# Kernel optimization log

Measured on AMD Instinct MI355X. Metric: run time of the kernel, lower is better.

The kernel has to match this reference:

```python
import jax, jax.numpy as jnp
import numpy as np

B, D, C = 8192, 256, 128
MARGIN = 0.5
REPULSION_WEIGHT = 1.0
ALPHA = 0.5
BETA = 0.5
EPS = 1e-6  # F.pairwise_distance default eps, added to the difference vector


def make_centers(num_classes=C, embedding_dim=D):
    # center[k] is +/-1 one-hot along axis (k % embedding_dim)
    idx = np.arange(num_classes)
    centers = np.zeros((num_classes, embedding_dim), dtype=np.float32)
    centers[idx, idx % embedding_dim] = np.where(idx % 2 == 0, 1.0, -1.0)
    return jnp.asarray(centers)


def setup_inputs() -> dict:
    key = jax.random.key(0)
    k1, k2, k3 = jax.random.split(key, 3)
    features = jax.random.normal(k1, (B, D), dtype=jnp.float32)
    classification = jax.random.normal(k2, (B, C), dtype=jnp.float32)
    labels = jax.random.randint(k3, (B,), 0, C, dtype=jnp.int32)
    return {"features": features, "classification": classification, "labels": labels}


def _sculpted_loss(embeddings, labels, centers):
    b = embeddings.shape[0]
    # attractive: MSE to per-sample class center, mean over all elements
    center_targets = centers[labels]  # [B, D]
    attractive = jnp.mean((embeddings - center_targets) ** 2)

    # repulsive: for pairs i<j with different labels,
    # relu(margin - ||e_i - e_j + eps||_2)^2, summed then / (B(B-1)/2).
    sq_norm = jnp.sum(embeddings ** 2, axis=1)          # [B]
    row_sum = jnp.sum(embeddings, axis=1)               # [B]
    gram = embeddings @ embeddings.T                    # [B, B]
    sq = (sq_norm[:, None] + sq_norm[None, :] - 2.0 * gram
          + 2.0 * EPS * (row_sum[:, None] - row_sum[None, :])
          + embeddings.shape[1] * (EPS * EPS))
    dist = jnp.sqrt(jnp.maximum(sq, 1e-12))             # [B, B]

    iu = jnp.triu(jnp.ones((b, b), dtype=bool), k=1)    # i < j
    diff_label = labels[:, None] != labels[None, :]
    mask = iu & diff_label
    hinge = jnp.maximum(MARGIN - dist, 0.0)
    repulsive = jnp.sum(jnp.where(mask, hinge * hinge, 0.0))
    repulsive = repulsive / (b * (b - 1) / 2.0)

    return attractive + REPULSION_WEIGHT * repulsive


def reference(features, classification, labels):
    centers = make_centers()
    # cross entropy (mean over batch)
    logp = jax.nn.log_softmax(classification, axis=-1)
    ce = -jnp.mean(jnp.take_along_axis(logp, labels[:, None].astype(jnp.int32), axis=1)[:, 0])
    contrastive = _sculpted_loss(features, labels, centers)
    return BETA * contrastive + ALPHA * ce
```

## Files before the change

kernel.cpp:

```cpp
#include <hip/hip_runtime.h>
#include <stdint.h>

#define B_N   8192
#define D_DIM 256
#define C_CLS 128
#define EPSV  1e-6f
#define DEPS  (256.0f * EPSV * EPSV)
#define NT    64
#define NTRI  (NT * (NT + 1) / 2)

typedef __bf16 bf16x8 __attribute__((ext_vector_type(8)));
typedef float  f32x4  __attribute__((ext_vector_type(4)));

__device__ __forceinline__ unsigned short f2bf(float v) {
    unsigned u = __float_as_uint(v);
    u += 0x7fff + ((u >> 16) & 1);
    return (unsigned short)(u >> 16);
}


__global__ __launch_bounds__(256) void k_prep(
        const float* __restrict__ feat, const float* __restrict__ cls,
        const int* __restrict__ labels, unsigned short* __restrict__ ebf,
        float* __restrict__ aR, float* __restrict__ bC,
        float* __restrict__ attrP, float* __restrict__ ceP) {
    int t = threadIdx.x, lane = t & 63, w = t >> 6;
    int row = blockIdx.x * 4 + w;
    int lab = labels[row];

    const float4* src = (const float4*)(feat + (size_t)row * D_DIM);
    float4 f = src[lane];
    ushort4 p;
    p.x = f2bf(f.x); p.y = f2bf(f.y); p.z = f2bf(f.z); p.w = f2bf(f.w);
    ((ushort4*)(ebf + (size_t)row * D_DIM))[lane] = p;

    float sq = f.x*f.x + f.y*f.y + f.z*f.z + f.w*f.w;
    float sm = f.x + f.y + f.z + f.w;
    float arr[4] = {f.x, f.y, f.z, f.w};
    float pick = ((lab >> 2) == lane) ? arr[lab & 3] : 0.f;

    const float2* csrc = (const float2*)(cls + (size_t)row * C_CLS);
    float2 c2 = csrc[lane];
    float mx = fmaxf(c2.x, c2.y);
    #pragma unroll
    for (int off = 32; off; off >>= 1) mx = fmaxf(mx, __shfl_xor(mx, off));
    float es = expf(c2.x - mx) + expf(c2.y - mx);
    float cpick = ((lab >> 1) == lane) ? ((lab & 1) ? c2.y : c2.x) : 0.f;

    #pragma unroll
    for (int off = 32; off; off >>= 1) {
        sq    += __shfl_xor(sq, off);
        sm    += __shfl_xor(sm, off);
        pick  += __shfl_xor(pick, off);
        es    += __shfl_xor(es, off);
        cpick += __shfl_xor(cpick, off);
    }
    __shared__ float wsumA[4], wsumC[4];
    if (lane == 0) {
        aR[row] = sq + 2.f * EPSV * sm;
        bC[row] = sq - 2.f * EPSV * sm + DEPS;
        float s = (lab & 1) ? -1.f : 1.f;
        wsumA[w] = sq - 2.f * s * pick + 1.f;
        wsumC[w] = -(cpick - mx - logf(es));
    }
    __syncthreads();
    if (t == 0) {
        attrP[blockIdx.x] = wsumA[0] + wsumA[1] + wsumA[2] + wsumA[3];
        ceP[blockIdx.x]   = wsumC[0] + wsumC[1] + wsumC[2] + wsumC[3];
    }
}

__global__ __launch_bounds__(256) void k_gram(
        const unsigned short* __restrict__ ebf, const float* __restrict__ aR,
        const float* __restrict__ bC, const int* __restrict__ labels,
        float* __restrict__ repP) {
    __shared__ __align__(16) unsigned short As[128 * 128];
    __shared__ __align__(16) unsigned short Bs[128 * 128];
    __shared__ float aM[128], bN[128];
    __shared__ int   lM[128], lN[128];
    __shared__ float wred[4];

    int t = threadIdx.x, lane = t & 63, w = t >> 6;

    int bid = blockIdx.x, tm = 0;
    while (bid >= NT - tm) { bid -= NT - tm; tm++; }
    int tn = tm + bid;

    if (t < 128) {
        int i = tm * 128 + t;
        aM[t] = aR[i]; lM[t] = labels[i];
    } else {
        int j = tn * 128 + (t - 128);
        bN[t - 128] = bC[j]; lN[t - 128] = labels[j];
    }

    f32x4 acc[4][4] = {};
    int wr = w >> 1, wc = w & 1;
    int srow = t >> 4;
    int scol = ((t & 15) ^ srow) * 8;
    int quad = lane >> 4, l15 = lane & 15;

    for (int k0 = 0; k0 < D_DIM; k0 += 128) {
        #pragma unroll
        for (int i = 0; i < 8; i++) {
            int row = i * 16 + srow;
            const unsigned short* ga = ebf + (size_t)(tm * 128 + row) * D_DIM + k0 + scol;
            const unsigned short* gb = ebf + (size_t)(tn * 128 + row) * D_DIM + k0 + scol;
            unsigned short* la = As + i * 2048 + (w * 64) * 8;
            unsigned short* lb = Bs + i * 2048 + (w * 64) * 8;
            __builtin_amdgcn_global_load_lds((const __attribute__((address_space(1))) void*)ga,
                                             (__attribute__((address_space(3))) void*)la, 16, 0, 0);
            __builtin_amdgcn_global_load_lds((const __attribute__((address_space(1))) void*)gb,
                                             (__attribute__((address_space(3))) void*)lb, 16, 0, 0);
        }
        __syncthreads();

        int m0 = wr * 64, n0 = wc * 64;
        #pragma unroll
        for (int kk = 0; kk < 128; kk += 32) {
            int kc = (kk >> 3) | quad;
            bf16x8 av[4], bv[4];
            #pragma unroll
            for (int mi = 0; mi < 4; mi++) {
                int r = m0 + mi * 16 + l15;
                av[mi] = *(const bf16x8*)(As + r * 128 + ((kc ^ l15) << 3));
            }
            #pragma unroll
            for (int ni = 0; ni < 4; ni++) {
                int r = n0 + ni * 16 + l15;
                bv[ni] = *(const bf16x8*)(Bs + r * 128 + ((kc ^ l15) << 3));
            }
            #pragma unroll
            for (int mi = 0; mi < 4; mi++)
                #pragma unroll
                for (int ni = 0; ni < 4; ni++)
                    acc[mi][ni] = __builtin_amdgcn_mfma_f32_16x16x32_bf16(av[mi], bv[ni], acc[mi][ni], 0, 0, 0);
        }
        __syncthreads();
    }

    float am[16], bn[4];
    #pragma unroll
    for (int ni = 0; ni < 4; ni++) bn[ni] = bN[wc * 64 + ni * 16 + l15];
    #pragma unroll
    for (int mi = 0; mi < 4; mi++)
        #pragma unroll
        for (int r = 0; r < 4; r++)
            am[mi * 4 + r] = aM[wr * 64 + mi * 16 + quad * 4 + r];

    float minv = 1e30f;
    #pragma unroll
    for (int mi = 0; mi < 4; mi++)
        #pragma unroll
        for (int ni = 0; ni < 4; ni++)
            #pragma unroll
            for (int r = 0; r < 4; r++)
                minv = fminf(minv, fmaf(-2.f, acc[mi][ni][r], am[mi * 4 + r] + bn[ni]));
    #pragma unroll
    for (int off = 32; off; off >>= 1) minv = fminf(minv, __shfl_xor(minv, off));

    float rep = 0.f;
    if (minv < 0.25f) {
        #pragma unroll
        for (int mi = 0; mi < 4; mi++) {
            #pragma unroll
            for (int ni = 0; ni < 4; ni++) {
                int n  = wc * 64 + ni * 16 + l15;
                int jg = tn * 128 + n;
                #pragma unroll
                for (int r = 0; r < 4; r++) {
                    int m  = wr * 64 + mi * 16 + quad * 4 + r;
                    int ig = tm * 128 + m;
                    float sq   = fmaf(-2.f, acc[mi][ni][r], am[mi * 4 + r] + bn[ni]);
                    float dist = sqrtf(fmaxf(sq, 1e-12f));
                    float h    = fmaxf(0.5f - dist, 0.f);
                    rep += (lM[m] != lN[n] && ig < jg) ? h * h : 0.f;
                }
            }
        }
        #pragma unroll
        for (int off = 32; off; off >>= 1) rep += __shfl_xor(rep, off);
    }
    if (lane == 0) wred[w] = rep;
    __syncthreads();
    if (t == 0) repP[blockIdx.x] = wred[0] + wred[1] + wred[2] + wred[3];
}

__global__ __launch_bounds__(256) void k_final(
        const float* __restrict__ P, float* __restrict__ out) {
    int t = threadIdx.x, lane = t & 63, w = t >> 6;
    float a = 0.f, c = 0.f, r = 0.f;
    for (int i = t; i < 2048; i += 256) { a += P[i]; c += P[2048 + i]; }
    for (int i = t; i < NTRI; i += 256) r += P[4096 + i];
    #pragma unroll
    for (int off = 32; off; off >>= 1) {
        a += __shfl_xor(a, off);
        c += __shfl_xor(c, off);
        r += __shfl_xor(r, off);
    }
    __shared__ float sa[4], sc[4], sr[4];
    if (lane == 0) { sa[w] = a; sc[w] = c; sr[w] = r; }
    __syncthreads();
    if (t == 0) {
        float attr = (sa[0] + sa[1] + sa[2] + sa[3]) / (float)((size_t)B_N * D_DIM);
        float ce   = (sc[0] + sc[1] + sc[2] + sc[3]) / (float)B_N;
        float rep  = (sr[0] + sr[1] + sr[2] + sr[3]) / ((float)B_N * (float)(B_N - 1) * 0.5f);
        out[0] = 0.5f * (attr + rep) + 0.5f * ce;
    }
}

extern "C" void kernel_launch(void* const* d_in, const int* in_sizes, int n_in,
                              void* d_out, int out_size, void* d_ws, size_t ws_size,
                              hipStream_t stream) {
    const float* feat   = (const float*)d_in[0];
    const float* cls    = (const float*)d_in[1];
    const int*   labels = (const int*)d_in[2];
    float* out = (float*)d_out;

    float*          P    = (float*)d_ws;
    unsigned short* ebf  = (unsigned short*)((char*)d_ws + 32768);
    float*          aR   = (float*)((char*)d_ws + 32768 + (size_t)B_N * D_DIM * 2);
    float*          bC   = aR + B_N;
    float*          attrP = P;
    float*          ceP   = P + 2048;
    float*          repP  = P + 4096;

    k_prep <<<2048, 256, 0, stream>>>(feat, cls, labels, ebf, aR, bC, attrP, ceP);
    k_gram <<<NTRI, 256, 0, stream>>>(ebf, aR, bC, labels, repP);
    k_final<<<1, 256, 0, stream>>>(P, out);
}
```

Measured before the change: 100.9 us.

## Quantize embeddings to FP8 and use FP8 MFMA for gram tiles

The embeddings are now quantized to FP8 (e4m3) in the prep kernel instead of bf16. The gram kernel loads the full 256-wide K dimension into LDS in a single pass and uses FP8 16x16x32 MFMA with 8-byte operand loads, with launch bounds raised to allow two blocks per CU. This halves the bytes loaded and roughly doubles MFMA throughput. The cost is much lower precision in the gram products, which feed a distance hinge at a 0.5 margin. Dot-product errors of this size could change the repulsive term, although the early-exit on min distance is usually taken for random data.

```diff
diff --git a/kernel.cpp b/kernel.cpp
--- a/kernel.cpp
+++ b/kernel.cpp
@@ -9,19 +9,23 @@
 #define NT    64
 #define NTRI  (NT * (NT + 1) / 2)
 
-typedef __bf16 bf16x8 __attribute__((ext_vector_type(8)));
-typedef float  f32x4  __attribute__((ext_vector_type(4)));
-
-__device__ __forceinline__ unsigned short f2bf(float v) {
+typedef float f32x4 __attribute__((ext_vector_type(4)));
+
+__device__ __forceinline__ unsigned f2fp8(float v) {
     unsigned u = __float_as_uint(v);
-    u += 0x7fff + ((u >> 16) & 1);
-    return (unsigned short)(u >> 16);
+    unsigned s = (u >> 24) & 0x80;
+    unsigned a = u & 0x7fffffff;
+    if (a > 0x43E00000u) a = 0x43E00000u;
+    a += 0x7FFFF + ((a >> 20) & 1);
+    int e = (int)(a >> 23) - 120;
+    if (e <= 0) return s;
+    return s | ((unsigned)e << 3) | ((a >> 20) & 7);
 }
 
 
 __global__ __launch_bounds__(256) void k_prep(
         const float* __restrict__ feat, const float* __restrict__ cls,
-        const int* __restrict__ labels, unsigned short* __restrict__ ebf,
+        const int* __restrict__ labels, unsigned char* __restrict__ e8,
         float* __restrict__ aR, float* __restrict__ bC,
         float* __restrict__ attrP, float* __restrict__ ceP) {
     int t = threadIdx.x, lane = t & 63, w = t >> 6;
@@ -30,9 +34,8 @@
 
     const float4* src = (const float4*)(feat + (size_t)row * D_DIM);
     float4 f = src[lane];
-    ushort4 p;
-    p.x = f2bf(f.x); p.y = f2bf(f.y); p.z = f2bf(f.z); p.w = f2bf(f.w);
-    ((ushort4*)(ebf + (size_t)row * D_DIM))[lane] = p;
+    unsigned pk = f2fp8(f.x) | (f2fp8(f.y) << 8) | (f2fp8(f.z) << 16) | (f2fp8(f.w) << 24);
+    ((unsigned*)(e8 + (size_t)row * D_DIM))[lane] = pk;
 
     float sq = f.x*f.x + f.y*f.y + f.z*f.z + f.w*f.w;
     float sm = f.x + f.y + f.z + f.w;
@@ -70,12 +73,12 @@
     }
 }
 
-__global__ __launch_bounds__(256) void k_gram(
-        const unsigned short* __restrict__ ebf, const float* __restrict__ aR,
+__global__ __launch_bounds__(256, 2) void k_gram(
+        const unsigned char* __restrict__ e8, const float* __restrict__ aR,
         const float* __restrict__ bC, const int* __restrict__ labels,
         float* __restrict__ repP) {
-    __shared__ __align__(16) unsigned short As[128 * 128];
-    __shared__ __align__(16) unsigned short Bs[128 * 128];
+    __shared__ __align__(16) unsigned char As[128 * 256];
+    __shared__ __align__(16) unsigned char Bs[128 * 256];
     __shared__ float aM[128], bN[128];
     __shared__ int   lM[128], lN[128];
     __shared__ float wred[4];
@@ -94,49 +97,47 @@
         bN[t - 128] = bC[j]; lN[t - 128] = labels[j];
     }
 
+    int srow = t >> 4;
+    int ulog = (lane & 15) ^ (srow & 15);
+    #pragma unroll
+    for (int i = 0; i < 8; i++) {
+        int row = i * 16 + srow;
+        const unsigned char* ga = e8 + (size_t)(tm * 128 + row) * D_DIM + ulog * 16;
+        const unsigned char* gb = e8 + (size_t)(tn * 128 + row) * D_DIM + ulog * 16;
+        unsigned char* la = As + i * 4096 + w * 1024;
+        unsigned char* lb = Bs + i * 4096 + w * 1024;
+        __builtin_amdgcn_global_load_lds((const __attribute__((address_space(1))) void*)ga,
+                                         (__attribute__((address_space(3))) void*)la, 16, 0, 0);
+        __builtin_amdgcn_global_load_lds((const __attribute__((address_space(1))) void*)gb,
+                                         (__attribute__((address_space(3))) void*)lb, 16, 0, 0);
+    }
+    __syncthreads();
+
     f32x4 acc[4][4] = {};
     int wr = w >> 1, wc = w & 1;
-    int srow = t >> 4;
-    int scol = ((t & 15) ^ srow) * 8;
     int quad = lane >> 4, l15 = lane & 15;
-
-    for (int k0 = 0; k0 < D_DIM; k0 += 128) {
-        #pragma unroll
-        for (int i = 0; i < 8; i++) {
-            int row = i * 16 + srow;
-            const unsigned short* ga = ebf + (size_t)(tm * 128 + row) * D_DIM + k0 + scol;
-            const unsigned short* gb = ebf + (size_t)(tn * 128 + row) * D_DIM + k0 + scol;
-            unsigned short* la = As + i * 2048 + (w * 64) * 8;
-            unsigned short* lb = Bs + i * 2048 + (w * 64) * 8;
-            __builtin_amdgcn_global_load_lds((const __attribute__((address_space(1))) void*)ga,
-                                             (__attribute__((address_space(3))) void*)la, 16, 0, 0);
-            __builtin_amdgcn_global_load_lds((const __attribute__((address_space(1))) void*)gb,
-                                             (__attribute__((address_space(3))) void*)lb, 16, 0, 0);
+    int m0 = wr * 64, n0 = wc * 64;
+    int half = (quad & 1) * 8, upair = quad >> 1;
+
+    #pragma unroll
+    for (int s = 0; s < 8; s++) {
+        int ul = s * 2 + upair;
+        long long av[4], bv[4];
+        #pragma unroll
+        for (int mi = 0; mi < 4; mi++) {
+            int m = m0 + mi * 16 + l15;
+            av[mi] = *(const long long*)(As + m * 256 + ((ul ^ l15) * 16) + half);
         }
-        __syncthreads();
-
-        int m0 = wr * 64, n0 = wc * 64;
-        #pragma unroll
-        for (int kk = 0; kk < 128; kk += 32) {
-            int kc = (kk >> 3) | quad;
-            bf16x8 av[4], bv[4];
+        #pragma unroll
+        for (int ni = 0; ni < 4; ni++) {
+            int n = n0 + ni * 16 + l15;
+            bv[ni] = *(const long long*)(Bs + n * 256 + ((ul ^ l15) * 16) + half);
+        }
+        #pragma unroll
+        for (int mi = 0; mi < 4; mi++)
             #pragma unroll
-            for (int mi = 0; mi < 4; mi++) {
-                int r = m0 + mi * 16 + l15;
-                av[mi] = *(const bf16x8*)(As + r * 128 + ((kc ^ l15) << 3));
-            }
-            #pragma unroll
-            for (int ni = 0; ni < 4; ni++) {
-                int r = n0 + ni * 16 + l15;
-                bv[ni] = *(const bf16x8*)(Bs + r * 128 + ((kc ^ l15) << 3));
-            }
-            #pragma unroll
-            for (int mi = 0; mi < 4; mi++)
-                #pragma unroll
-                for (int ni = 0; ni < 4; ni++)
-                    acc[mi][ni] = __builtin_amdgcn_mfma_f32_16x16x32_bf16(av[mi], bv[ni], acc[mi][ni], 0, 0, 0);
-        }
-        __syncthreads();
+            for (int ni = 0; ni < 4; ni++)
+                acc[mi][ni] = __builtin_amdgcn_mfma_f32_16x16x32_fp8_fp8(av[mi], bv[ni], acc[mi][ni], 0, 0, 0);
     }
 
     float am[16], bn[4];
@@ -218,14 +219,14 @@
     float* out = (float*)d_out;
 
     float*          P    = (float*)d_ws;
-    unsigned short* ebf  = (unsigned short*)((char*)d_ws + 32768);
-    float*          aR   = (float*)((char*)d_ws + 32768 + (size_t)B_N * D_DIM * 2);
+    unsigned char*  e8   = (unsigned char*)d_ws + 32768;
+    float*          aR   = (float*)((char*)d_ws + 32768 + (size_t)B_N * D_DIM);
     float*          bC   = aR + B_N;
     float*          attrP = P;
     float*          ceP   = P + 2048;
     float*          repP  = P + 4096;
 
-    k_prep <<<2048, 256, 0, stream>>>(feat, cls, labels, ebf, aR, bC, attrP, ceP);
-    k_gram <<<NTRI, 256, 0, stream>>>(ebf, aR, bC, labels, repP);
+    k_prep <<<2048, 256, 0, stream>>>(feat, cls, labels, e8, aR, bC, attrP, ceP);
+    k_gram <<<NTRI, 256, 0, stream>>>(e8, aR, bC, labels, repP);
     k_final<<<1, 256, 0, stream>>>(P, out);
 }
```

Result: no change. 99.26 us (-1.6%).
